# Performance work log

Measured on AMD Instinct MI355X. Metric: run time of the kernel, lower is better.

Reference implementation:

```python
import jax, jax.numpy as jnp
import numpy as np

N_NODES = 32000
N_EDGES = 512000
F_IN = 128
HEADS = 4
CH = 64
NODES_PER_GRAPH = 500
BATCH = 64
HID = 512
ZDIM = 64


def _gat_layer(x, src, dst, W, att_src, att_dst, bias):
    # PyG GATConv, concat=True, negative_slope=0.2, self-loops already appended.
    N = x.shape[0]
    h = (x @ W).reshape(N, HEADS, CH)                 # [N,H,C]
    a_s = jnp.sum(h * att_src, axis=-1)               # [N,H]
    a_d = jnp.sum(h * att_dst, axis=-1)               # [N,H]
    e = jax.nn.leaky_relu(a_s[src] + a_d[dst], negative_slope=0.2)  # [E,H]
    m = jax.ops.segment_max(e, dst, num_segments=N)   # segment softmax over dst
    p = jnp.exp(e - m[dst])
    denom = jax.ops.segment_sum(p, dst, num_segments=N)
    alpha = p / denom[dst]                            # [E,H]
    out = jax.ops.segment_sum(h[src] * alpha[..., None], dst, num_segments=N)
    return out.reshape(N, HEADS * CH) + bias


def setup_inputs() -> dict:
    key = jax.random.key(0)
    ks = jax.random.split(key, 16)
    s = 0.02
    x = jax.random.normal(ks[0], (N_NODES, F_IN), jnp.float32)
    edge_index = jax.random.randint(ks[1], (2, N_EDGES), 0, N_NODES, jnp.int64)
    W1 = jax.random.normal(ks[2], (F_IN, HEADS * CH), jnp.float32) * s
    att_src1 = jax.random.normal(ks[3], (HEADS, CH), jnp.float32) * s
    att_dst1 = jax.random.normal(ks[4], (HEADS, CH), jnp.float32) * s
    b1 = jnp.zeros((HEADS * CH,), jnp.float32)
    W2 = jax.random.normal(ks[5], (HEADS * CH, HEADS * CH), jnp.float32) * s
    att_src2 = jax.random.normal(ks[6], (HEADS, CH), jnp.float32) * s
    att_dst2 = jax.random.normal(ks[7], (HEADS, CH), jnp.float32) * s
    b2 = jnp.zeros((HEADS * CH,), jnp.float32)
    We = jax.random.normal(ks[8], (NODES_PER_GRAPH * HEADS * CH, HID), jnp.float32) * 0.002
    be = jnp.zeros((HID,), jnp.float32)
    Wmu = jax.random.normal(ks[9], (HID, ZDIM), jnp.float32) * s
    bmu = jnp.zeros((ZDIM,), jnp.float32)
    Wvar = jax.random.normal(ks[10], (HID, ZDIM), jnp.float32) * s
    bvar = jnp.zeros((ZDIM,), jnp.float32)
    return {"x": x, "W1": W1, "att_src1": att_src1, "att_dst1": att_dst1, "b1": b1,
            "W2": W2, "att_src2": att_src2, "att_dst2": att_dst2, "b2": b2,
            "We": We, "be": be, "Wmu": Wmu, "bmu": bmu, "Wvar": Wvar, "bvar": bvar,
            "edge_index": edge_index, "batch": BATCH}


def reference(x, W1, att_src1, att_dst1, b1, W2, att_src2, att_dst2, b2,
              We, be, Wmu, bmu, Wvar, bvar, edge_index, batch):
    N = x.shape[0]
    loops = jnp.arange(N, dtype=edge_index.dtype)
    src = jnp.concatenate([edge_index[0], loops])
    dst = jnp.concatenate([edge_index[1], loops])
    h = jax.nn.relu(_gat_layer(x, src, dst, W1, att_src1, att_dst1, b1))
    h = jax.nn.relu(_gat_layer(h, src, dst, W2, att_src2, att_dst2, b2))
    xg = h.reshape(batch, -1)                         # [B, in_fea*H*C]
    y = xg @ We + be                                  # [B, HID]
    mu_b = jnp.mean(y, axis=0)                        # BatchNorm1d (training stats), eps=1e-3
    var_b = jnp.var(y, axis=0)
    y = (y - mu_b) / jnp.sqrt(var_b + 1e-3)
    mu_l = jnp.mean(y, axis=-1, keepdims=True)        # LayerNorm, no affine, eps=1e-5
    var_l = jnp.var(y, axis=-1, keepdims=True)
    y = (y - mu_l) / jnp.sqrt(var_l + 1e-5)
    y = jax.nn.relu(y)
    z_loc = y @ Wmu + bmu
    z_scale = jnp.exp(y @ Wvar + bvar) + 1e-4
    return (z_loc, z_scale)
```

## Files before the change

kernel.cpp:

```cpp
#include <hip/hip_runtime.h>
#include <math.h>

#define NN 32000
#define FIN 128
#define HC 256
#define NH 4
#define HIDD 512
#define BB 64
#define ZD 64
#define NSPLIT 250
#define KBCH 512
#define BNB 128

typedef __bf16 bf16x8 __attribute__((ext_vector_type(8)));
typedef float f32x4 __attribute__((ext_vector_type(4)));
typedef unsigned int uint;

__device__ inline float lrelu(float x){ return x > 0.f ? x : 0.2f*x; }
__device__ inline unsigned short f2b(float f){
  uint u = __float_as_uint(f);
  return (unsigned short)((u + 0x7FFFu + ((u >> 16) & 1u)) >> 16);
}
__device__ inline float b2f(unsigned short b){ return __uint_as_float(((uint)b) << 16); }
__device__ inline float blo(uint v){ return __uint_as_float(v << 16); }
__device__ inline float bhi(uint v){ return __uint_as_float(v & 0xffff0000u); }
__device__ inline uint cvtpk(float lo, float hi){
  uint pk;
  asm("v_cvt_pk_bf16_f32 %0, %1, %2" : "=v"(pk) : "v"(lo), "v"(hi));
  return pk;
}

__global__ void k_prep0(const void* ei, int* flag, int* counts){
  int b = blockIdx.x, t = threadIdx.x;
  if (b == 0 && t < 64){
    int v = ((const int*)ei)[2*t + 1];
    unsigned long long bal = __ballot(v == 0);
    if (t == 0) *flag = (bal == ~0ULL) ? 1 : 0;
  }
  for (int i = b*256 + t; i < NN; i += gridDim.x*256) counts[i] = 0;
}

__global__ void k_prep1(const float* __restrict__ x, unsigned short* __restrict__ xb,
                        const float* __restrict__ W1, unsigned short* __restrict__ Wt1,
                        const float* __restrict__ W2, unsigned short* __restrict__ Wt2,
                        const void* ei, const int* __restrict__ flag,
                        int* __restrict__ counts, int E){
  int b = blockIdx.x, t = threadIdx.x;
  if (b < 16000){
    int i = b*256 + t;
    xb[i] = f2b(x[i]);
  } else if (b < 16512){
    int bb = b - 16000;
    int n = bb & 255, which = bb >> 8;
    if (which == 0){ if (t < FIN) Wt1[n*FIN + t] = f2b(W1[t*HC + n]); }
    else           { Wt2[n*HC + t] = f2b(W2[t*HC + n]); }
  } else {
    int i = (b - 16512)*256 + t;
    if (i < E){
      int d = *flag ? (int)((const long long*)ei)[E + i] : ((const int*)ei)[E + i];
      atomicAdd(&counts[d], 1);
    }
  }
}

__global__ __launch_bounds__(256) void k_scanA(const int* __restrict__ counts,
                                               int* __restrict__ bsum){
  __shared__ int red[256];
  int b = blockIdx.x, t = threadIdx.x;
  red[t] = counts[b*256 + t];
  __syncthreads();
  #pragma unroll
  for (int o = 128; o; o >>= 1){
    if (t < o) red[t] += red[t + o];
    __syncthreads();
  }
  if (t == 0) bsum[b] = red[0];
}

__global__ __launch_bounds__(128) void k_scanB(int* __restrict__ bsum, int nb){
  __shared__ int s[128];
  int t = threadIdx.x;
  int v = (t < nb) ? bsum[t] : 0;
  s[t] = v;
  __syncthreads();
  for (int o = 1; o < 128; o <<= 1){
    int u = (t >= o) ? s[t - o] : 0;
    __syncthreads();
    s[t] += u;
    __syncthreads();
  }
  if (t < nb) bsum[t] = s[t] - v;
}

__global__ __launch_bounds__(256) void k_scanC(const int* __restrict__ counts,
    const int* __restrict__ bsum, int* __restrict__ offs, int* __restrict__ cursor){
  __shared__ int s[256];
  int b = blockIdx.x, t = threadIdx.x;
  int v = counts[b*256 + t];
  s[t] = v;
  __syncthreads();
  for (int o = 1; o < 256; o <<= 1){
    int u = (t >= o) ? s[t - o] : 0;
    __syncthreads();
    s[t] += u;
    __syncthreads();
  }
  int excl = s[t] - v + bsum[b];
  offs[b*256 + t] = excl;
  cursor[b*256 + t] = excl;
  if (b == (NN/256 - 1) && t == 255) offs[NN] = excl + v;
}

__global__ void k_fill(const void* ei, const int* __restrict__ flag,
                       int* __restrict__ cursor, int* __restrict__ col, int E){
  int i = blockIdx.x*256 + threadIdx.x;
  if (i < E){
    int s, d;
    if (*flag){ s = (int)((const long long*)ei)[i]; d = (int)((const long long*)ei)[E + i]; }
    else      { s = ((const int*)ei)[i];            d = ((const int*)ei)[E + i]; }
    int pos = atomicAdd(&cursor[d], 1);
    col[pos] = s;
  }
}

__global__ __launch_bounds__(256) void k_gemm_n(const unsigned short* __restrict__ A,
    const unsigned short* __restrict__ Wt, int K,
    const float* __restrict__ ws, const float* __restrict__ wd,
    unsigned short* __restrict__ out, float* __restrict__ a_s, float* __restrict__ a_d){
  __shared__ unsigned short As[64][40];
  __shared__ unsigned short Bs[256][40];
  int m0 = blockIdx.x * 64;
  int t = threadIdx.x;
  int w = t >> 6, lane = t & 63, l15 = lane & 15, l16 = lane >> 4;
  f32x4 acc[16];
  #pragma unroll
  for (int c = 0; c < 16; c++) acc[c] = (f32x4){0.f,0.f,0.f,0.f};

  for (int k0 = 0; k0 < K; k0 += 32){
    {
      int row = t >> 2, ko = (t & 3) * 8;
      *(uint4*)&As[row][ko] = *(const uint4*)&A[(size_t)(m0 + row)*K + k0 + ko];
    }
    {
      #pragma unroll
      for (int p = 0; p < 4; p++)
        *(uint4*)&Bs[t][p*8] = *(const uint4*)&Wt[(size_t)t*K + k0 + p*8];
    }
    __syncthreads();
    bf16x8 af = *(const bf16x8*)&As[w*16 + l15][l16*8];
    #pragma unroll
    for (int c = 0; c < 16; c++){
      bf16x8 bfr = *(const bf16x8*)&Bs[c*16 + l15][l16*8];
      acc[c] = __builtin_amdgcn_mfma_f32_16x16x32_bf16(af, bfr, acc[c], 0, 0, 0);
    }
    __syncthreads();
  }

  #pragma unroll
  for (int r = 0; r < 4; r++){
    int row = m0 + w*16 + l16*4 + r;
    float hs[NH] = {0,0,0,0}, hd[NH] = {0,0,0,0};
    #pragma unroll
    for (int c = 0; c < 16; c++){
      float v = acc[c][r];
      int colc = c*16 + l15;
      out[(size_t)row*HC + colc] = f2b(v);
      hs[c>>2] += v * ws[colc];
      hd[c>>2] += v * wd[colc];
    }
    #pragma unroll
    for (int h = 0; h < NH; h++){
      float s = hs[h], d = hd[h];
      #pragma unroll
      for (int o = 1; o < 16; o <<= 1){ s += __shfl_xor(s, o); d += __shfl_xor(d, o); }
      if (l15 == h){ a_s[row*NH + h] = s; a_d[row*NH + h] = d; }
    }
  }
}

__global__ __launch_bounds__(256) void k_agg(const unsigned short* __restrict__ hp,
    const int* __restrict__ col, const int* __restrict__ offs,
    const float* __restrict__ a_s, const float* __restrict__ a_d,
    const float* __restrict__ bias, unsigned short* __restrict__ outb){
  int n = blockIdx.x*4 + (threadIdx.x >> 6);
  int lane = threadIdx.x & 63;
  int g = lane >> 4, l16 = lane & 15;
  int h = l16 >> 2;
  int c0 = l16 * 16;
  int b0 = offs[n], b1 = offs[n+1];
  float adh = a_d[n*NH + h];
  float pself = expf(lrelu(a_s[n*NH + h] + adh));
  float den = 0.f;
  float ac[16];
  #pragma unroll
  for (int j = 0; j < 16; j++) ac[j] = 0.f;
  #pragma unroll 2
  for (int i = b0 + g; i < b1; i += 4){
    int s = col[i];
    float p = expf(lrelu(a_s[s*NH + h] + adh));
    den += p;
    uint4 v0 = *(const uint4*)&hp[(size_t)s*HC + c0];
    uint4 v1 = *(const uint4*)&hp[(size_t)s*HC + c0 + 8];
    ac[0] = fmaf(p, blo(v0.x), ac[0]);   ac[1] = fmaf(p, bhi(v0.x), ac[1]);
    ac[2] = fmaf(p, blo(v0.y), ac[2]);   ac[3] = fmaf(p, bhi(v0.y), ac[3]);
    ac[4] = fmaf(p, blo(v0.z), ac[4]);   ac[5] = fmaf(p, bhi(v0.z), ac[5]);
    ac[6] = fmaf(p, blo(v0.w), ac[6]);   ac[7] = fmaf(p, bhi(v0.w), ac[7]);
    ac[8] = fmaf(p, blo(v1.x), ac[8]);   ac[9] = fmaf(p, bhi(v1.x), ac[9]);
    ac[10]= fmaf(p, blo(v1.y), ac[10]);  ac[11]= fmaf(p, bhi(v1.y), ac[11]);
    ac[12]= fmaf(p, blo(v1.z), ac[12]);  ac[13]= fmaf(p, bhi(v1.z), ac[13]);
    ac[14]= fmaf(p, blo(v1.w), ac[14]);  ac[15]= fmaf(p, bhi(v1.w), ac[15]);
  }
  den += __shfl_xor(den, 16);  den += __shfl_xor(den, 32);
  #pragma unroll
  for (int j = 0; j < 16; j++){
    ac[j] += __shfl_xor(ac[j], 16);
    ac[j] += __shfl_xor(ac[j], 32);
  }
  den += pself;
  float r = 1.f / den;
  if (g == 0){
    uint4 hv0 = *(const uint4*)&hp[(size_t)n*HC + c0];
    uint4 hv1 = *(const uint4*)&hp[(size_t)n*HC + c0 + 8];
    float hvf[16] = {blo(hv0.x),bhi(hv0.x),blo(hv0.y),bhi(hv0.y),
                     blo(hv0.z),bhi(hv0.z),blo(hv0.w),bhi(hv0.w),
                     blo(hv1.x),bhi(hv1.x),blo(hv1.y),bhi(hv1.y),
                     blo(hv1.z),bhi(hv1.z),blo(hv1.w),bhi(hv1.w)};
    uint ov[8];
    #pragma unroll
    for (int j = 0; j < 8; j++){
      float e0 = fmaxf((pself*hvf[2*j]   + ac[2*j]  )*r + bias[c0+2*j],   0.f);
      float e1 = fmaxf((pself*hvf[2*j+1] + ac[2*j+1])*r + bias[c0+2*j+1], 0.f);
      ov[j] = ((uint)f2b(e1) << 16) | (uint)f2b(e0);
    }
    *(uint4*)&outb[(size_t)n*HC + c0]     = *(uint4*)&ov[0];
    *(uint4*)&outb[(size_t)n*HC + c0 + 8] = *(uint4*)&ov[4];
  }
}

__global__ __launch_bounds__(256) void k_gemm_big(const unsigned short* __restrict__ xg,
    const float* __restrict__ We, float* __restrict__ part){
  __shared__ unsigned short As[2][64][40];
  __shared__ unsigned short Bs[2][BNB][40];
  int n0 = blockIdx.x * BNB;
  int kc = blockIdx.y;
  int kbase = kc * KBCH;
  int t = threadIdx.x, w = t >> 6, lane = t & 63, l15 = lane & 15, l16 = lane >> 4;
  int cc = t & (BNB-1);
  int khalf = t >> 7;
  int arow = t >> 2, ako = (t & 3) * 8;
  const float* bptr = We + (size_t)(kbase + khalf*16)*HIDD + n0 + cc;
  const unsigned short* aptr = xg + (size_t)arow*128000 + kbase + ako;
  f32x4 acc[8];
  #pragma unroll
  for (int c = 0; c < 8; c++) acc[c] = (f32x4){0.f,0.f,0.f,0.f};

  float rv[16]; uint4 a4;
  #pragma unroll
  for (int mm = 0; mm < 16; mm++) rv[mm] = bptr[(size_t)mm*HIDD];
  a4 = *(const uint4*)aptr;

  int p = 0;
  for (int ks = 0; ks < KBCH; ks += 32){
    *(uint4*)&As[p][arow][ako] = a4;
    #pragma unroll
    for (int j = 0; j < 8; j++)
      *(uint*)&Bs[p][cc][khalf*16 + 2*j] = cvtpk(rv[2*j], rv[2*j+1]);
    __syncthreads();
    if (ks + 32 < KBCH){
      const float* bp2 = bptr + (size_t)(ks + 32)*HIDD;
      #pragma unroll
      for (int mm = 0; mm < 16; mm++) rv[mm] = bp2[(size_t)mm*HIDD];
      a4 = *(const uint4*)(aptr + ks + 32);
    }
    bf16x8 af = *(const bf16x8*)&As[p][w*16 + l15][l16*8];
    #pragma unroll
    for (int c = 0; c < 8; c++){
      bf16x8 bfr = *(const bf16x8*)&Bs[p][c*16 + l15][l16*8];
      acc[c] = __builtin_amdgcn_mfma_f32_16x16x32_bf16(af, bfr, acc[c], 0, 0, 0);
    }
    p ^= 1;
  }
  float* pbase = part + (size_t)kc*BB*HIDD;
  #pragma unroll
  for (int r = 0; r < 4; r++){
    int row = w*16 + l16*4 + r;
    #pragma unroll
    for (int c = 0; c < 8; c++)
      pbase[row*HIDD + n0 + c*16 + l15] = acc[c][r];
  }
}

__global__ void k_reduce(const float* __restrict__ part, const float* __restrict__ be,
                         float* __restrict__ y){
  int o = blockIdx.x*256 + threadIdx.x;
  float s = 0.f;
  #pragma unroll 5
  for (int k = 0; k < NSPLIT; k++) s += part[(size_t)k*BB*HIDD + o];
  y[o] = s + be[o & (HIDD-1)];
}

__global__ __launch_bounds__(64) void k_bn(const float* __restrict__ y,
    float* __restrict__ ybn){
  int colb = blockIdx.x, r = threadIdx.x;
  float v = y[(size_t)r*HIDD + colb];
  float s = v, s2 = v*v;
  #pragma unroll
  for (int o = 32; o; o >>= 1){ s += __shfl_down(s, o); s2 += __shfl_down(s2, o); }
  s = __shfl(s, 0); s2 = __shfl(s2, 0);
  float mean = s * (1.f/BB);
  float var = s2 * (1.f/BB) - mean*mean;
  ybn[(size_t)r*HIDD + colb] = (v - mean) * rsqrtf(var + 1e-3f);
}

__global__ __launch_bounds__(512) void k_lnheads(const float* __restrict__ ybn,
    const float* __restrict__ Wmu, const float* __restrict__ bmu,
    const float* __restrict__ Wvar, const float* __restrict__ bvar,
    float* __restrict__ out){
  __shared__ float ssum[8], ssq[8];
  __shared__ float yrow[HIDD];
  int row = blockIdx.x, t = threadIdx.x;
  float v = ybn[(size_t)row*HIDD + t];
  float s = v, s2 = v*v;
  #pragma unroll
  for (int o = 32; o; o >>= 1){ s += __shfl_down(s, o); s2 += __shfl_down(s2, o); }
  if ((t & 63) == 0){ ssum[t>>6] = s; ssq[t>>6] = s2; }
  __syncthreads();
  if (t == 0){
    float S = 0, S2 = 0;
    for (int i = 0; i < 8; i++){ S += ssum[i]; S2 += ssq[i]; }
    ssum[0] = S; ssq[0] = S2;
  }
  __syncthreads();
  float mean = ssum[0] * (1.f/HIDD);
  float var = ssq[0] * (1.f/HIDD) - mean*mean;
  yrow[t] = fmaxf((v - mean) * rsqrtf(var + 1e-5f), 0.f);
  __syncthreads();
  int o = t >> 2, kq = t & 3;
  const float* Wc = (o < ZD) ? Wmu : Wvar;
  int j = (o < ZD) ? o : o - ZD;
  float acc = 0.f;
  #pragma unroll 4
  for (int k = kq*128; k < kq*128 + 128; k++)
    acc = fmaf(yrow[k], Wc[(size_t)k*ZD + j], acc);
  acc += __shfl_down(acc, 1);
  acc += __shfl_down(acc, 2);
  if (kq == 0){
    if (o < ZD) out[row*ZD + o] = acc + bmu[o];
    else        out[BB*ZD + row*ZD + j] = expf(acc + bvar[j]) + 1e-4f;
  }
}

extern "C" void kernel_launch(void* const* d_in, const int* in_sizes, int n_in,
                              void* d_out, int out_size, void* d_ws, size_t ws_size,
                              hipStream_t stream){
  const float* x    = (const float*)d_in[0];
  const float* W1   = (const float*)d_in[1];
  const float* as1  = (const float*)d_in[2];
  const float* ad1  = (const float*)d_in[3];
  const float* b1   = (const float*)d_in[4];
  const float* W2   = (const float*)d_in[5];
  const float* as2  = (const float*)d_in[6];
  const float* ad2  = (const float*)d_in[7];
  const float* b2   = (const float*)d_in[8];
  const float* We   = (const float*)d_in[9];
  const float* be   = (const float*)d_in[10];
  const float* Wmu  = (const float*)d_in[11];
  const float* bmu  = (const float*)d_in[12];
  const float* Wvar = (const float*)d_in[13];
  const float* bvar = (const float*)d_in[14];
  const void*  ei   = d_in[15];
  int E = in_sizes[15] / 2;

  char* w = (char*)d_ws;
  auto alloc = [&](size_t bytes)->void*{
    void* p = (void*)w; w += (bytes + 255) & ~(size_t)255; return p;
  };
  unsigned short* gb   = (unsigned short*)alloc((size_t)NN*HC*2);
  unsigned short* ab   = (unsigned short*)alloc((size_t)NN*HC*2);
  unsigned short* xb   = (unsigned short*)alloc((size_t)NN*FIN*2);
  unsigned short* Wt1  = (unsigned short*)alloc((size_t)HC*FIN*2);
  unsigned short* Wt2  = (unsigned short*)alloc((size_t)HC*HC*2);
  float*    a_s    = (float*)alloc((size_t)NN*NH*4);
  float*    a_d    = (float*)alloc((size_t)NN*NH*4);
  int*      counts = (int*)alloc((size_t)NN*4);
  int*      offs   = (int*)alloc((size_t)(NN+1)*4);
  int*      cursor = (int*)alloc((size_t)NN*4);
  int*      col    = (int*)alloc((size_t)E*4);
  int*      bsum   = (int*)alloc((size_t)256*4);
  int*      flag   = (int*)alloc(256);
  float*    part   = (float*)alloc((size_t)NSPLIT*BB*HIDD*4);
  float*    y      = (float*)alloc((size_t)BB*HIDD*4);
  float*    ybn    = (float*)alloc((size_t)BB*HIDD*4);

  k_prep0<<<125, 256, 0, stream>>>(ei, flag, counts);
  k_prep1<<<16512 + (E + 255)/256, 256, 0, stream>>>(x, xb, W1, Wt1, W2, Wt2,
                                                     ei, flag, counts, E);
  k_scanA<<<NN/256, 256, 0, stream>>>(counts, bsum);
  k_scanB<<<1, 128, 0, stream>>>(bsum, NN/256);
  k_scanC<<<NN/256, 256, 0, stream>>>(counts, bsum, offs, cursor);
  k_fill<<<(E + 255)/256, 256, 0, stream>>>(ei, flag, cursor, col, E);

  k_gemm_n<<<NN/64, 256, 0, stream>>>(xb, Wt1, FIN, as1, ad1, gb, a_s, a_d);
  k_agg<<<NN/4, 256, 0, stream>>>(gb, col, offs, a_s, a_d, b1, ab);

  k_gemm_n<<<NN/64, 256, 0, stream>>>(ab, Wt2, HC, as2, ad2, gb, a_s, a_d);
  k_agg<<<NN/4, 256, 0, stream>>>(gb, col, offs, a_s, a_d, b2, ab);

  k_gemm_big<<<dim3(HIDD/BNB, NSPLIT), 256, 0, stream>>>(ab, We, part);
  k_reduce<<<BB*HIDD/256, 256, 0, stream>>>(part, be, y);
  k_bn<<<HIDD, 64, 0, stream>>>(y, ybn);
  k_lnheads<<<BB, 512, 0, stream>>>(ybn, Wmu, bmu, Wvar, bvar, (float*)d_out);
}
```

Before: 289.4 us.

## Double-buffer GEMM LDS tiles, vectorize x bf16 cast, halve big-GEMM split count

The node GEMM now double-buffers its LDS tiles. The next K-slice is prefetched into registers during the MFMA loop, and one barrier per iteration is dropped. The x-to-bf16 conversion handles four floats per thread with packed convert instructions, which cuts the number of blocks in the prep kernel. The big encoder GEMM's K-split count is halved and its chunk size doubled, so fewer partial sums need reducing, at the cost of less parallelism per output.

```diff
diff --git a/kernel.cpp b/kernel.cpp
--- a/kernel.cpp
+++ b/kernel.cpp
@@ -8,8 +8,8 @@
 #define HIDD 512
 #define BB 64
 #define ZD 64
-#define NSPLIT 250
-#define KBCH 512
+#define NSPLIT 125
+#define KBCH 1024
 #define BNB 128
 
 typedef __bf16 bf16x8 __attribute__((ext_vector_type(8)));
@@ -46,16 +46,19 @@
                         const void* ei, const int* __restrict__ flag,
                         int* __restrict__ counts, int E){
   int b = blockIdx.x, t = threadIdx.x;
-  if (b < 16000){
-    int i = b*256 + t;
-    xb[i] = f2b(x[i]);
-  } else if (b < 16512){
-    int bb = b - 16000;
+  if (b < 4000){
+    int i = b*1024 + t*4;
+    float4 v = *(const float4*)&x[i];
+    uint p0 = cvtpk(v.x, v.y), p1 = cvtpk(v.z, v.w);
+    uint2 o; o.x = p0; o.y = p1;
+    *(uint2*)&xb[i] = o;
+  } else if (b < 4512){
+    int bb = b - 4000;
     int n = bb & 255, which = bb >> 8;
     if (which == 0){ if (t < FIN) Wt1[n*FIN + t] = f2b(W1[t*HC + n]); }
     else           { Wt2[n*HC + t] = f2b(W2[t*HC + n]); }
   } else {
-    int i = (b - 16512)*256 + t;
+    int i = (b - 4512)*256 + t;
     if (i < E){
       int d = *flag ? (int)((const long long*)ei)[E + i] : ((const int*)ei)[E + i];
       atomicAdd(&counts[d], 1);
@@ -127,33 +130,41 @@
     const unsigned short* __restrict__ Wt, int K,
     const float* __restrict__ ws, const float* __restrict__ wd,
     unsigned short* __restrict__ out, float* __restrict__ a_s, float* __restrict__ a_d){
-  __shared__ unsigned short As[64][40];
-  __shared__ unsigned short Bs[256][40];
+  __shared__ unsigned short As[2][64][40];
+  __shared__ unsigned short Bs[2][256][40];
   int m0 = blockIdx.x * 64;
   int t = threadIdx.x;
   int w = t >> 6, lane = t & 63, l15 = lane & 15, l16 = lane >> 4;
+  int arow = t >> 2, ako = (t & 3) * 8;
+  const unsigned short* aptr = A + (size_t)(m0 + arow)*K + ako;
+  const unsigned short* bptr = Wt + (size_t)t*K;
   f32x4 acc[16];
   #pragma unroll
   for (int c = 0; c < 16; c++) acc[c] = (f32x4){0.f,0.f,0.f,0.f};
 
+  uint4 a4 = *(const uint4*)aptr;
+  uint4 b4[4];
+  #pragma unroll
+  for (int p = 0; p < 4; p++) b4[p] = *(const uint4*)(bptr + p*8);
+
+  int pp = 0;
   for (int k0 = 0; k0 < K; k0 += 32){
-    {
-      int row = t >> 2, ko = (t & 3) * 8;
-      *(uint4*)&As[row][ko] = *(const uint4*)&A[(size_t)(m0 + row)*K + k0 + ko];
-    }
-    {
+    *(uint4*)&As[pp][arow][ako] = a4;
+    #pragma unroll
+    for (int p = 0; p < 4; p++) *(uint4*)&Bs[pp][t][p*8] = b4[p];
+    __syncthreads();
+    if (k0 + 32 < K){
+      a4 = *(const uint4*)(aptr + k0 + 32);
       #pragma unroll
-      for (int p = 0; p < 4; p++)
-        *(uint4*)&Bs[t][p*8] = *(const uint4*)&Wt[(size_t)t*K + k0 + p*8];
-    }
-    __syncthreads();
-    bf16x8 af = *(const bf16x8*)&As[w*16 + l15][l16*8];
+      for (int p = 0; p < 4; p++) b4[p] = *(const uint4*)(bptr + k0 + 32 + p*8);
+    }
+    bf16x8 af = *(const bf16x8*)&As[pp][w*16 + l15][l16*8];
     #pragma unroll
     for (int c = 0; c < 16; c++){
-      bf16x8 bfr = *(const bf16x8*)&Bs[c*16 + l15][l16*8];
+      bf16x8 bfr = *(const bf16x8*)&Bs[pp][c*16 + l15][l16*8];
       acc[c] = __builtin_amdgcn_mfma_f32_16x16x32_bf16(af, bfr, acc[c], 0, 0, 0);
     }
-    __syncthreads();
+    pp ^= 1;
   }
 
   #pragma unroll
@@ -393,8 +404,8 @@
   float*    ybn    = (float*)alloc((size_t)BB*HIDD*4);
 
   k_prep0<<<125, 256, 0, stream>>>(ei, flag, counts);
-  k_prep1<<<16512 + (E + 255)/256, 256, 0, stream>>>(x, xb, W1, Wt1, W2, Wt2,
-                                                     ei, flag, counts, E);
+  k_prep1<<<4512 + (E + 255)/256, 256, 0, stream>>>(x, xb, W1, Wt1, W2, Wt2,
+                                                    ei, flag, counts, E);
   k_scanA<<<NN/256, 256, 0, stream>>>(counts, bsum);
   k_scanB<<<1, 128, 0, stream>>>(bsum, NN/256);
   k_scanC<<<NN/256, 256, 0, stream>>>(counts, bsum, offs, cursor);
```

New measurement: 288.5 us (median of 2 runs). No clear change (-0.3%).
